# Kernel tuning notes

Hardware: AMD Instinct MI355X
Metric: run time of the kernel (lower is better)

The kernel has to match this reference:

```python
import jax, jax.numpy as jnp
import numpy as np

# Dimensions
B, D1, D2 = 256, 68, 3          # inputs: [B, 68 landmarks, 3 coords]
OUT = D1 * D2                   # output_size = 204
H = 1024                        # hidden_size
NUM_CLASSES = 12
LENGTH = 128                    # decoded sequence length
NUM_LAYERS = 3
IN0 = OUT + NUM_CLASSES         # LSTM layer-0 input size = 216


def setup_inputs() -> dict:
    key = jax.random.key(0)
    ks = jax.random.split(key, 32)
    s = 0.02

    def rn(k, shape):
        return (jax.random.normal(k, shape, jnp.float32) * s)

    inp = {
        "inputs": jax.random.normal(ks[0], (B, D1, D2), jnp.float32),
        # LSTM layer 0 (input size IN0), layers 1,2 (input size H). Gate order: i,f,g,o.
        "W_ih0": rn(ks[1], (IN0, 4 * H)), "W_hh0": rn(ks[2], (H, 4 * H)),
        "b_ih0": rn(ks[3], (4 * H,)),     "b_hh0": rn(ks[4], (4 * H,)),
        "W_ih1": rn(ks[5], (H, 4 * H)),   "W_hh1": rn(ks[6], (H, 4 * H)),
        "b_ih1": rn(ks[7], (4 * H,)),     "b_hh1": rn(ks[8], (4 * H,)),
        "W_ih2": rn(ks[9], (H, 4 * H)),   "W_hh2": rn(ks[10], (H, 4 * H)),
        "b_ih2": rn(ks[11], (4 * H,)),    "b_hh2": rn(ks[12], (4 * H,)),
        # fc head: hidden -> output_size
        "fc_W": rn(ks[13], (H, OUT)), "fc_b": rn(ks[14], (OUT,)),
        # state initializers: output_size -> 3*hidden
        "inh_W": rn(ks[15], (OUT, 3 * H)), "inh_b": rn(ks[16], (3 * H,)),
        "inc_W": rn(ks[17], (OUT, 3 * H)), "inc_b": rn(ks[18], (3 * H,)),
        "labels": 5,  # scalar class id
    }
    return inp


def _lstm_cell(x, h, c, W_ih, W_hh, b_ih, b_hh):
    gates = x @ W_ih + h @ W_hh + (b_ih + b_hh)        # [B, 4H]
    i, f, g, o = jnp.split(gates, 4, axis=-1)
    i = jax.nn.sigmoid(i)
    f = jax.nn.sigmoid(f)
    g = jnp.tanh(g)
    o = jax.nn.sigmoid(o)
    c2 = f * c + i * g
    h2 = o * jnp.tanh(c2)
    return h2, c2


def reference(inputs, W_ih0, W_hh0, b_ih0, b_hh0,
              W_ih1, W_hh1, b_ih1, b_hh1,
              W_ih2, W_hh2, b_ih2, b_hh2,
              fc_W, fc_b, inh_W, inh_b, inc_W, inc_b, labels):
    b, d1, d2 = inputs.shape
    frame = inputs.reshape(b, d1 * d2)                              # [B, OUT]
    # init states, reshaped (B, 3, H) -> (layers, B, H)
    h0 = (frame @ inh_W + inh_b).reshape(b, NUM_LAYERS, H).transpose(1, 0, 2)
    c0 = (frame @ inc_W + inc_b).reshape(b, NUM_LAYERS, H).transpose(1, 0, 2)
    enc = jax.nn.one_hot(jnp.asarray(labels), NUM_CLASSES, dtype=frame.dtype)
    x_in = jnp.concatenate([frame, jnp.broadcast_to(enc, (b, NUM_CLASSES))], axis=-1)  # [B, IN0]

    layers = ((W_ih0, W_hh0, b_ih0, b_hh0),
              (W_ih1, W_hh1, b_ih1, b_hh1),
              (W_ih2, W_hh2, b_ih2, b_hh2))

    def step(carry, _):
        h, c = carry                                                # each [3, B, H]
        x = x_in
        hs, cs = [], []
        for l in range(NUM_LAYERS):
            hn, cn = _lstm_cell(x, h[l], c[l], *layers[l])
            hs.append(hn)
            cs.append(cn)
            x = hn
        out = x @ fc_W + fc_b                                       # [B, OUT]
        return (jnp.stack(hs), jnp.stack(cs)), out

    (_, _), outs = jax.lax.scan(step, (h0, c0), None, length=LENGTH)  # [L, B, OUT]
    return outs.transpose(1, 0, 2).reshape(b, LENGTH, d1, d2)
```

## Files before the change

kernel.cpp:

```cpp
#include <hip/hip_runtime.h>


#define DEVINL static __device__ __forceinline__

typedef __bf16 bf16x8 __attribute__((ext_vector_type(8)));
typedef float f32x4 __attribute__((ext_vector_type(4)));
typedef unsigned short u16;
typedef unsigned int u32;

DEVINL u16 f2bf(float f) {
  u32 u = __builtin_bit_cast(u32, f);
  u += 0x7fffu + ((u >> 16) & 1u);
  return (u16)(u >> 16);
}
DEVINL float bf2f(u16 h) {
  u32 u = (u32)h << 16;
  return __builtin_bit_cast(float, u);
}
DEVINL float sigm(float x) { return 1.0f / (1.0f + __expf(-x)); }
DEVINL float tanhfast(float x) { return 1.0f - 2.0f / (1.0f + __expf(2.0f * x)); }

DEVINL void glds_coh(const u16* g, u16* l) {
  __builtin_amdgcn_global_load_lds(
      (const __attribute__((address_space(1))) u32*)g,
      (__attribute__((address_space(3))) u32*)l, 16, 0, 17);
}
DEVINL void glds(const u16* g, u16* l) {
  __builtin_amdgcn_global_load_lds(
      (const __attribute__((address_space(1))) u32*)g,
      (__attribute__((address_space(3))) u32*)l, 16, 0, 0);
}

DEVINL int permcol(int P) {
  int grp = P >> 6, g = (P >> 4) & 3, jj = P & 15;
  return g * 1024 + grp * 16 + jj;
}

struct Params {
  const float* fc_b;
  const float* inh_b;
  const float* inc_b;
  const u16 *WT0, *WT1, *WT2, *WT00, *FCW, *WIH, *WIC, *FRB;
  u16* HB;
  u16* G0P;
  float *G0B, *B1P, *B2P, *CC;
  float* out;
};

#define MODE_L0 0
#define MODE_L 1
#define MODE_FC 2
#define MODE_G0 3
#define MODE_H 4
#define MODE_C 5

DEVINL void issue_tile(int kt, const u16* A0, const u16* A1, int kSplit, int sA,
                       int K, const u16* Wt, int m0, int wrow,
                       const int (&rq)[4], const int (&kqs)[4],
                       const int (&lo)[4], u16* Abuf, u16* Bbuf) {
  const u16* Ab = (kt < kSplit) ? (A0 + kt) : (A1 + (kt - kSplit));
#pragma unroll
  for (int q = 0; q < 4; ++q)
    glds_coh(Ab + (size_t)(m0 + rq[q]) * sA + kqs[q] * 8, Abuf + lo[q]);
  const u16* Bb = Wt + kt;
#pragma unroll
  for (int q = 0; q < 2; ++q)
    glds(Bb + (size_t)(wrow + rq[q]) * K + kqs[q] * 8, Bbuf + lo[q]);
}

DEVINL void mfma_tile(const u16* Al, const u16* Bl, f32x4 (&acc)[2][4], int rl0,
                      int hh, int e7, int jj) {
#pragma unroll
  for (int kk = 0; kk < 2; ++kk) {
    int sl = (((kk << 2) | hh) ^ e7) * 8;
    bf16x8 a0 = *(const bf16x8*)(Al + rl0 * 64 + sl);
    bf16x8 a1 = *(const bf16x8*)(Al + (rl0 + 16) * 64 + sl);
    bf16x8 b0 = *(const bf16x8*)(Bl + (jj)*64 + sl);
    bf16x8 b1 = *(const bf16x8*)(Bl + (16 + jj) * 64 + sl);
    bf16x8 b2 = *(const bf16x8*)(Bl + (32 + jj) * 64 + sl);
    bf16x8 b3 = *(const bf16x8*)(Bl + (48 + jj) * 64 + sl);
    acc[0][0] = __builtin_amdgcn_mfma_f32_16x16x32_bf16(a0, b0, acc[0][0], 0, 0, 0);
    acc[0][1] = __builtin_amdgcn_mfma_f32_16x16x32_bf16(a0, b1, acc[0][1], 0, 0, 0);
    acc[0][2] = __builtin_amdgcn_mfma_f32_16x16x32_bf16(a0, b2, acc[0][2], 0, 0, 0);
    acc[0][3] = __builtin_amdgcn_mfma_f32_16x16x32_bf16(a0, b3, acc[0][3], 0, 0, 0);
    acc[1][0] = __builtin_amdgcn_mfma_f32_16x16x32_bf16(a1, b0, acc[1][0], 0, 0, 0);
    acc[1][1] = __builtin_amdgcn_mfma_f32_16x16x32_bf16(a1, b1, acc[1][1], 0, 0, 0);
    acc[1][2] = __builtin_amdgcn_mfma_f32_16x16x32_bf16(a1, b2, acc[1][2], 0, 0, 0);
    acc[1][3] = __builtin_amdgcn_mfma_f32_16x16x32_bf16(a1, b3, acc[1][3], 0, 0, 0);
  }
}

template <int MODE>
DEVINL void mm_body(u16* Al, u16* Bl, const u16* A0, const u16* A1, int sA,
                    int kSplit, int K, const u16* Wt, int m0, int bn, int t,
                    const u16* Gfull, const float* biasP, float* Cst, u16* Hout,
                    float* outp) {
  const int tid = threadIdx.x;
  const int l = tid & 63;
  const int w = tid >> 6;
  const int hh = (l >> 4) & 3;
  const int jj = l & 15;
  const int rl0 = w * 32 + jj;
  const int e7 = l & 7;

  int rq[4], kqs[4], lo[4];
#pragma unroll
  for (int q = 0; q < 4; ++q) {
    int L = tid + q * 256;
    rq[q] = L >> 3;
    kqs[q] = (L & 7) ^ (rq[q] & 7);
    lo[q] = ((tid & ~63) + q * 256) * 8;
  }

  f32x4 acc[2][4];
#pragma unroll
  for (int m = 0; m < 2; ++m)
#pragma unroll
    for (int g = 0; g < 4; ++g) acc[m][g] = (f32x4){0.f, 0.f, 0.f, 0.f};

  const int wrow = bn * 64;
  const int n = K >> 6;

  issue_tile(0, A0, A1, kSplit, sA, K, Wt, m0, wrow, rq, kqs, lo, Al, Bl);
  issue_tile(64, A0, A1, kSplit, sA, K, Wt, m0, wrow, rq, kqs, lo, Al + 8192,
             Bl + 4096);

  for (int j = 0; j < n; ++j) {
    u16* Ac = Al + (j & 1) * 8192;
    u16* Bc = Bl + (j & 1) * 4096;
    if (j < n - 1)
      asm volatile("s_waitcnt vmcnt(6)" ::: "memory");
    else
      asm volatile("s_waitcnt vmcnt(0)" ::: "memory");
    __builtin_amdgcn_s_barrier();
    __builtin_amdgcn_sched_barrier(0);
    mfma_tile(Ac, Bc, acc, rl0, hh, e7, jj);
    __builtin_amdgcn_sched_barrier(0);
    __builtin_amdgcn_s_barrier();
    if (j + 2 < n)
      issue_tile((j + 2) * 64, A0, A1, kSplit, sA, K, Wt, m0, wrow, rq, kqs, lo,
                 Ac, Bc);
  }

  const int rb = m0 + w * 32 + (hh << 2);
  if (MODE <= MODE_L) {
    float add0 = 0.f, add1 = 0.f, add2 = 0.f, add3 = 0.f;
    if (MODE == MODE_L) {
      add0 = biasP[bn * 64 + jj];
      add1 = biasP[bn * 64 + 16 + jj];
      add2 = biasP[bn * 64 + 32 + jj];
      add3 = biasP[bn * 64 + 48 + jj];
    }
    const int j = bn * 16 + jj;
#pragma unroll
    for (int m = 0; m < 2; ++m) {
#pragma unroll
      for (int r = 0; r < 4; ++r) {
        int b = rb + m * 16 + r;
        float g0v, g1v, g2v, g3v;
        if (MODE == MODE_L0) {
          const u16* G = Gfull + (size_t)b * 4096 + bn * 64 + jj;
          g0v = acc[m][0][r] + bf2f(G[0]);
          g1v = acc[m][1][r] + bf2f(G[16]);
          g2v = acc[m][2][r] + bf2f(G[32]);
          g3v = acc[m][3][r] + bf2f(G[48]);
        } else {
          g0v = acc[m][0][r] + add0;
          g1v = acc[m][1][r] + add1;
          g2v = acc[m][2][r] + add2;
          g3v = acc[m][3][r] + add3;
        }
        float iv = sigm(g0v), fv = sigm(g1v), gv = tanhfast(g2v), ov = sigm(g3v);
        size_t ci = (size_t)b * 1024 + j;
        float cn = fv * Cst[ci] + iv * gv;
        Cst[ci] = cn;
        Hout[ci] = f2bf(ov * tanhfast(cn));
      }
    }
  } else if (MODE == MODE_FC) {
#pragma unroll
    for (int g = 0; g < 4; ++g) {
      int nn = bn * 64 + g * 16 + jj;
      if (nn < 204) {
        float bv2 = biasP[nn];
#pragma unroll
        for (int m = 0; m < 2; ++m)
#pragma unroll
          for (int r = 0; r < 4; ++r) {
            int b = rb + m * 16 + r;
            outp[((size_t)b * 128 + t) * 204 + nn] = acc[m][g][r] + bv2;
          }
      }
    }
  } else if (MODE == MODE_G0) {
#pragma unroll
    for (int g = 0; g < 4; ++g) {
      int P = bn * 64 + g * 16 + jj;
      float bv2 = biasP[P];
#pragma unroll
      for (int m = 0; m < 2; ++m)
#pragma unroll
        for (int r = 0; r < 4; ++r) {
          int b = rb + m * 16 + r;
          Hout[(size_t)b * 4096 + P] = f2bf(acc[m][g][r] + bv2);
        }
    }
  } else {
#pragma unroll
    for (int g = 0; g < 4; ++g) {
      int nn = bn * 64 + g * 16 + jj;
      int lay = nn >> 10, j2 = nn & 1023;
      float bv2 = biasP[nn];
#pragma unroll
      for (int m = 0; m < 2; ++m)
#pragma unroll
        for (int r = 0; r < 4; ++r) {
          int b = rb + m * 16 + r;
          float v = acc[m][g][r] + bv2;
          if (MODE == MODE_H)
            Hout[(size_t)((lay * 2 + 1) * 256 + b) * 1024 + j2] = f2bf(v);
          else
            outp[(size_t)(lay * 256 + b) * 1024 + j2] = v;
        }
    }
  }
}

DEVINL void grid_barrier(u32* bar, int bid, int ep) {
  __syncthreads();
  if (threadIdx.x == 0) {
    __builtin_amdgcn_fence(__ATOMIC_RELEASE, "agent");
    __hip_atomic_fetch_add(bar + (bid & 7) * 64, 1u, __ATOMIC_RELAXED,
                           __HIP_MEMORY_SCOPE_AGENT);
    if (bid == 0) {
#pragma unroll 1
      for (int g = 0; g < 8; ++g)
        while (__hip_atomic_load(bar + g * 64, __ATOMIC_RELAXED,
                                 __HIP_MEMORY_SCOPE_AGENT) < (u32)ep * 49u)
          __builtin_amdgcn_s_sleep(8);
      __hip_atomic_store(bar + 512, (u32)ep, __ATOMIC_RELAXED,
                         __HIP_MEMORY_SCOPE_AGENT);
    } else {
#pragma unroll 1
      while (__hip_atomic_load(bar + 512, __ATOMIC_RELAXED,
                               __HIP_MEMORY_SCOPE_AGENT) < (u32)ep)
        __builtin_amdgcn_s_sleep(8);
    }
  }
  __syncthreads();
}

__global__ __launch_bounds__(256, 2) void persist_kernel(Params p, u32* bar) {
  __shared__ u16 Al[2 * 128 * 64];
  __shared__ u16 Bl[2 * 64 * 64];
  const int bid = blockIdx.x;
  int job, mb, bn;
  if (bid < 384) {
    job = bid >> 7;
    int r = bid & 127;
    bn = (r & 7) * 8 + (r >> 4);
    mb = (r >> 3) & 1;
  } else {
    job = 3;
    int r = bid - 384;
    mb = r >> 2;
    bn = r & 3;
  }
  u16* HB = p.HB;
#define HBP(lay, pp) (HB + (size_t)(((lay)*2 + (pp)) * 256) * 1024)
  for (int i = 0; i <= 130; ++i) {
    int t = i - job;
    if ((unsigned)t < 128u) {
      int par = t & 1, pv = par ^ 1;
      if (job == 0) {
        mm_body<MODE_L0>(Al, Bl, HBP(0, pv), nullptr, 1024, 1 << 30, 1024,
                         p.WT0, mb * 128, bn, t, p.G0P, nullptr, p.CC,
                         HBP(0, par), nullptr);
      } else if (job == 1) {
        mm_body<MODE_L>(Al, Bl, HBP(0, par), HBP(1, pv), 1024, 1024, 2048,
                        p.WT1, mb * 128, bn, t, nullptr, p.B1P,
                        p.CC + (size_t)256 * 1024, HBP(1, par), nullptr);
      } else if (job == 2) {
        mm_body<MODE_L>(Al, Bl, HBP(1, par), HBP(2, pv), 1024, 1024, 2048,
                        p.WT2, mb * 128, bn, t, nullptr, p.B2P,
                        p.CC + (size_t)512 * 1024, HBP(2, par), nullptr);
      } else {
        mm_body<MODE_FC>(Al, Bl, HBP(2, par), nullptr, 1024, 1 << 30, 1024,
                         p.FCW, mb * 128, bn, t, nullptr, p.fc_b, nullptr,
                         nullptr, p.out);
      }
    }
    if (i < 130) grid_barrier(bar, bid, i + 1);
  }
#undef HBP
}

__global__ __launch_bounds__(256, 2) void setup_mm(Params p) {
  __shared__ u16 Al[2 * 128 * 64];
  __shared__ u16 Bl[2 * 64 * 64];
  int bid = blockIdx.x;
  if (bid < 128) {
    mm_body<MODE_G0>(Al, Bl, p.FRB, nullptr, 256, 1 << 30, 256, p.WT00,
                     (bid >> 6) * 128, bid & 63, 0, nullptr, p.G0B, nullptr,
                     p.G0P, nullptr);
  } else if (bid < 224) {
    int b2 = bid - 128;
    mm_body<MODE_H>(Al, Bl, p.FRB, nullptr, 256, 1 << 30, 256, p.WIH,
                    (b2 / 48) * 128, b2 % 48, 0, nullptr, p.inh_b, nullptr,
                    p.HB, nullptr);
  } else {
    int b2 = bid - 224;
    mm_body<MODE_C>(Al, Bl, p.FRB, nullptr, 256, 1 << 30, 256, p.WIC,
                    (b2 / 48) * 128, b2 % 48, 0, nullptr, p.inc_b, nullptr,
                    nullptr, p.CC);
  }
}

__global__ __launch_bounds__(256) void transpose_bf16(
    const float* __restrict__ srcA, const float* __restrict__ srcB,
    int srcStride, int kSplit, int Kvalid, int Nvalid, int perm,
    u16* __restrict__ dst, int Ktot) {
  __shared__ float tile[64][17];
  int P0 = blockIdx.x * 16;
  int k0 = blockIdx.y * 64;
  int t = threadIdx.x;
  int nl = t & 15;
  int kh = t >> 4;
  int P = P0 + nl;
  int n = perm ? permcol(P) : P;
  bool nok = (n < Nvalid);
#pragma unroll
  for (int q = 0; q < 4; ++q) {
    int kl = q * 16 + kh;
    int k = k0 + kl;
    float v = 0.f;
    if (nok && k < Kvalid) {
      const float* s = (k < kSplit) ? (srcA + (size_t)k * srcStride)
                                    : (srcB + (size_t)(k - kSplit) * srcStride);
      v = s[n];
    }
    tile[kl][nl] = v;
  }
  __syncthreads();
  int jo = t >> 4;
  int kb = (t & 15) << 2;
  unsigned long long pk =
      (unsigned long long)f2bf(tile[kb + 0][jo]) |
      ((unsigned long long)f2bf(tile[kb + 1][jo]) << 16) |
      ((unsigned long long)f2bf(tile[kb + 2][jo]) << 32) |
      ((unsigned long long)f2bf(tile[kb + 3][jo]) << 48);
  *(unsigned long long*)(dst + (size_t)(P0 + jo) * Ktot + k0 + kb) = pk;
}

__global__ __launch_bounds__(256) void build_frame(const float* __restrict__ inputs,
                                                   u16* __restrict__ FRB) {
  int id = blockIdx.x * 256 + threadIdx.x;
  int b = id >> 8, k = id & 255;
  FRB[id] = (k < 204) ? f2bf(inputs[b * 204 + k]) : (u16)0;
}

__global__ __launch_bounds__(256) void build_bias(
    const float* __restrict__ W_ih0, const float* __restrict__ b_ih0,
    const float* __restrict__ b_hh0, const float* __restrict__ b_ih1,
    const float* __restrict__ b_hh1, const float* __restrict__ b_ih2,
    const float* __restrict__ b_hh2, const int* __restrict__ labels,
    float* __restrict__ G0B, float* __restrict__ B1P, float* __restrict__ B2P) {
  int P = blockIdx.x * 256 + threadIdx.x;
  int n = permcol(P);
  int lab = labels[0];
  G0B[P] = W_ih0[(size_t)(204 + lab) * 4096 + n] + b_ih0[n] + b_hh0[n];
  B1P[P] = b_ih1[n] + b_hh1[n];
  B2P[P] = b_ih2[n] + b_hh2[n];
}

extern "C" void kernel_launch(void* const* d_in, const int* in_sizes, int n_in,
                              void* d_out, int out_size, void* d_ws,
                              size_t ws_size, hipStream_t stream) {
  const float* inputs = (const float*)d_in[0];
  const float* W_ih0 = (const float*)d_in[1];
  const float* W_hh0 = (const float*)d_in[2];
  const float* b_ih0 = (const float*)d_in[3];
  const float* b_hh0 = (const float*)d_in[4];
  const float* W_ih1 = (const float*)d_in[5];
  const float* W_hh1 = (const float*)d_in[6];
  const float* b_ih1 = (const float*)d_in[7];
  const float* b_hh1 = (const float*)d_in[8];
  const float* W_ih2 = (const float*)d_in[9];
  const float* W_hh2 = (const float*)d_in[10];
  const float* b_ih2 = (const float*)d_in[11];
  const float* b_hh2 = (const float*)d_in[12];
  const float* fc_W = (const float*)d_in[13];
  const float* fc_b = (const float*)d_in[14];
  const float* inh_W = (const float*)d_in[15];
  const float* inh_b = (const float*)d_in[16];
  const float* inc_W = (const float*)d_in[17];
  const float* inc_b = (const float*)d_in[18];
  const int* labels = (const int*)d_in[19];

  char* ws = (char*)d_ws;
  size_t off = 0;
  auto alloc = [&](size_t bytes) {
    void* r = ws + off;
    off = (off + bytes + 255) & ~(size_t)255;
    return r;
  };
  u16* WT0 = (u16*)alloc(4096ull * 1024 * 2);
  u16* WT1 = (u16*)alloc(4096ull * 2048 * 2);
  u16* WT2 = (u16*)alloc(4096ull * 2048 * 2);
  u16* WT00 = (u16*)alloc(4096ull * 256 * 2);
  u16* FCW = (u16*)alloc(256ull * 1024 * 2);
  u16* WIH = (u16*)alloc(3072ull * 256 * 2);
  u16* WIC = (u16*)alloc(3072ull * 256 * 2);
  u16* FRB = (u16*)alloc(256ull * 256 * 2);
  u16* HB = (u16*)alloc(3ull * 2 * 256 * 1024 * 2);
  u16* G0P = (u16*)alloc(256ull * 4096 * 2);
  float* G0B = (float*)alloc(4096ull * 4);
  float* B1P = (float*)alloc(4096ull * 4);
  float* B2P = (float*)alloc(4096ull * 4);
  float* CC = (float*)alloc(3ull * 256 * 1024 * 4);
  u32* BAR = (u32*)alloc(4096);
  if (off > ws_size) return;

  const int BIG = 1 << 30;
  transpose_bf16<<<dim3(256, 16), 256, 0, stream>>>(W_hh0, nullptr, 4096, BIG, 1024, 4096, 1, WT0, 1024);
  transpose_bf16<<<dim3(256, 32), 256, 0, stream>>>(W_ih1, W_hh1, 4096, 1024, 2048, 4096, 1, WT1, 2048);
  transpose_bf16<<<dim3(256, 32), 256, 0, stream>>>(W_ih2, W_hh2, 4096, 1024, 2048, 4096, 1, WT2, 2048);
  transpose_bf16<<<dim3(256, 4), 256, 0, stream>>>(W_ih0, nullptr, 4096, BIG, 204, 4096, 1, WT00, 256);
  transpose_bf16<<<dim3(16, 16), 256, 0, stream>>>(fc_W, nullptr, 204, BIG, 1024, 204, 0, FCW, 1024);
  transpose_bf16<<<dim3(192, 4), 256, 0, stream>>>(inh_W, nullptr, 3072, BIG, 204, 3072, 0, WIH, 256);
  transpose_bf16<<<dim3(192, 4), 256, 0, stream>>>(inc_W, nullptr, 3072, BIG, 204, 3072, 0, WIC, 256);
  build_frame<<<256, 256, 0, stream>>>(inputs, FRB);
  build_bias<<<16, 256, 0, stream>>>(W_ih0, b_ih0, b_hh0, b_ih1, b_hh1, b_ih2,
                                     b_hh2, labels, G0B, B1P, B2P);
  hipMemsetAsync(BAR, 0, 4096, stream);

  Params p;
  p.fc_b = fc_b; p.inh_b = inh_b; p.inc_b = inc_b;
  p.WT0 = WT0; p.WT1 = WT1; p.WT2 = WT2; p.WT00 = WT00; p.FCW = FCW;
  p.WIH = WIH; p.WIC = WIC; p.FRB = FRB; p.HB = HB;
  p.G0P = G0P; p.G0B = G0B; p.B1P = B1P; p.B2P = B2P; p.CC = CC;
  p.out = (float*)d_out;

  setup_mm<<<320, 256, 0, stream>>>(p);

  persist_kernel<<<392, 256, 0, stream>>>(p, BAR);
}
```

Before: 5.285 ms.

## Mirror hidden states per XCD so GEMM A-loads hit local L2

Each XCD's blocks first copy the full previous-step hidden-state buffers (all three layers) into a private per-XCD mirror, using coherent atomic loads, and then sync with a new XCD-local barrier. The GEMM A-operand loads then read from the mirror through cacheable loads instead of the system-coherent loads used before. The aim is to avoid slow cross-XCD coherent traffic on the repeated A-tile reads. The cost is an extra copy of about 1.5MB per XCD every step, an extra barrier per step, and dependence on the hardware XCC id register for grouping blocks.

```diff
diff --git a/kernel.cpp b/kernel.cpp
--- a/kernel.cpp
+++ b/kernel.cpp
@@ -7,6 +7,7 @@
 typedef float f32x4 __attribute__((ext_vector_type(4)));
 typedef unsigned short u16;
 typedef unsigned int u32;
+typedef unsigned long long u64;
 
 DEVINL u16 f2bf(float f) {
   u32 u = __builtin_bit_cast(u32, f);
@@ -20,12 +21,12 @@
 DEVINL float sigm(float x) { return 1.0f / (1.0f + __expf(-x)); }
 DEVINL float tanhfast(float x) { return 1.0f - 2.0f / (1.0f + __expf(2.0f * x)); }
 
-DEVINL void glds_coh(const u16* g, u16* l) {
+DEVINL void glds_a(const u16* g, u16* l) {
   __builtin_amdgcn_global_load_lds(
       (const __attribute__((address_space(1))) u32*)g,
-      (__attribute__((address_space(3))) u32*)l, 16, 0, 17);
-}
-DEVINL void glds(const u16* g, u16* l) {
+      (__attribute__((address_space(3))) u32*)l, 16, 0, 1);
+}
+DEVINL void glds_w(const u16* g, u16* l) {
   __builtin_amdgcn_global_load_lds(
       (const __attribute__((address_space(1))) u32*)g,
       (__attribute__((address_space(3))) u32*)l, 16, 0, 0);
@@ -42,6 +43,7 @@
   const float* inc_b;
   const u16 *WT0, *WT1, *WT2, *WT00, *FCW, *WIH, *WIC, *FRB;
   u16* HB;
+  u16* HM;
   u16* G0P;
   float *G0B, *B1P, *B2P, *CC;
   float* out;
@@ -61,11 +63,11 @@
   const u16* Ab = (kt < kSplit) ? (A0 + kt) : (A1 + (kt - kSplit));
 #pragma unroll
   for (int q = 0; q < 4; ++q)
-    glds_coh(Ab + (size_t)(m0 + rq[q]) * sA + kqs[q] * 8, Abuf + lo[q]);
+    glds_a(Ab + (size_t)(m0 + rq[q]) * sA + kqs[q] * 8, Abuf + lo[q]);
   const u16* Bb = Wt + kt;
 #pragma unroll
   for (int q = 0; q < 2; ++q)
-    glds(Bb + (size_t)(wrow + rq[q]) * K + kqs[q] * 8, Bbuf + lo[q]);
+    glds_w(Bb + (size_t)(wrow + rq[q]) * K + kqs[q] * 8, Bbuf + lo[q]);
 }
 
 DEVINL void mfma_tile(const u16* Al, const u16* Bl, f32x4 (&acc)[2][4], int rl0,
@@ -250,9 +252,37 @@
   __syncthreads();
 }
 
+DEVINL void xcd_barrier(u32* ctr, int nb, int ep) {
+  __syncthreads();
+  if (threadIdx.x == 0) {
+    __hip_atomic_fetch_add(ctr, 1u, __ATOMIC_RELAXED, __HIP_MEMORY_SCOPE_AGENT);
+#pragma unroll 1
+    while (__hip_atomic_load(ctr, __ATOMIC_RELAXED, __HIP_MEMORY_SCOPE_AGENT) <
+           (u32)ep * (u32)nb)
+      __builtin_amdgcn_s_sleep(4);
+  }
+  __syncthreads();
+}
+
+DEVINL void pull_mirror(const u16* HB, u16* HMx, int i, int rank, int nb) {
+  const int total = 3 * 65536;
+  const int stride = nb * 256;
+  u64* dst = (u64*)HMx;
+#pragma unroll 4
+  for (int c = rank * 256 + threadIdx.x; c < total; c += stride) {
+    int lyr = c >> 16, off = c & 65535;
+    int pl = (i - 1 - lyr) & 1;
+    const u64* s = (const u64*)(HB + ((size_t)(lyr * 2 + pl) << 18));
+    u64 v = __hip_atomic_load(s + off, __ATOMIC_RELAXED,
+                              __HIP_MEMORY_SCOPE_AGENT);
+    dst[c] = v;
+  }
+}
+
 __global__ __launch_bounds__(256, 2) void persist_kernel(Params p, u32* bar) {
   __shared__ u16 Al[2 * 128 * 64];
   __shared__ u16 Bl[2 * 64 * 64];
+  __shared__ int sh_x, sh_rank, sh_nb;
   const int bid = blockIdx.x;
   int job, mb, bn;
   if (bid < 384) {
@@ -266,31 +296,57 @@
     mb = r >> 2;
     bn = r & 3;
   }
+
+  if (threadIdx.x == 0) {
+    int x = __builtin_amdgcn_s_getreg((31 << 11) | 20) & 7;
+    sh_x = x;
+    sh_rank = (int)__hip_atomic_fetch_add(bar + 1024 + x * 64, 1u,
+                                          __ATOMIC_RELAXED,
+                                          __HIP_MEMORY_SCOPE_AGENT);
+  }
+  __syncthreads();
+  const int x = sh_x, rank = sh_rank;
+  grid_barrier(bar, bid, 1);
+  if (threadIdx.x == 0)
+    sh_nb = (int)__hip_atomic_load(bar + 1024 + x * 64, __ATOMIC_RELAXED,
+                                   __HIP_MEMORY_SCOPE_AGENT);
+  __syncthreads();
+  const int nb = sh_nb;
+  u16* HMx = p.HM + ((size_t)(x * 3) << 18);
+  u32* xctr = bar + 2048 + x * 64;
+
+  pull_mirror(p.HB, HMx, 0, rank, nb);
+  xcd_barrier(xctr, nb, 1);
+
   u16* HB = p.HB;
-#define HBP(lay, pp) (HB + (size_t)(((lay)*2 + (pp)) * 256) * 1024)
+#define HBP(lay, pp) (HB + (size_t)(((lay)*2 + (pp)) << 18))
   for (int i = 0; i <= 130; ++i) {
     int t = i - job;
     if ((unsigned)t < 128u) {
-      int par = t & 1, pv = par ^ 1;
+      int par = t & 1;
       if (job == 0) {
-        mm_body<MODE_L0>(Al, Bl, HBP(0, pv), nullptr, 1024, 1 << 30, 1024,
-                         p.WT0, mb * 128, bn, t, p.G0P, nullptr, p.CC,
-                         HBP(0, par), nullptr);
+        mm_body<MODE_L0>(Al, Bl, HMx, nullptr, 1024, 1 << 30, 1024, p.WT0,
+                         mb * 128, bn, t, p.G0P, nullptr, p.CC, HBP(0, par),
+                         nullptr);
       } else if (job == 1) {
-        mm_body<MODE_L>(Al, Bl, HBP(0, par), HBP(1, pv), 1024, 1024, 2048,
-                        p.WT1, mb * 128, bn, t, nullptr, p.B1P,
+        mm_body<MODE_L>(Al, Bl, HMx, HMx + (1 << 18), 1024, 1024, 2048, p.WT1,
+                        mb * 128, bn, t, nullptr, p.B1P,
                         p.CC + (size_t)256 * 1024, HBP(1, par), nullptr);
       } else if (job == 2) {
-        mm_body<MODE_L>(Al, Bl, HBP(1, par), HBP(2, pv), 1024, 1024, 2048,
-                        p.WT2, mb * 128, bn, t, nullptr, p.B2P,
+        mm_body<MODE_L>(Al, Bl, HMx + (1 << 18), HMx + (2 << 18), 1024, 1024,
+                        2048, p.WT2, mb * 128, bn, t, nullptr, p.B2P,
                         p.CC + (size_t)512 * 1024, HBP(2, par), nullptr);
       } else {
-        mm_body<MODE_FC>(Al, Bl, HBP(2, par), nullptr, 1024, 1 << 30, 1024,
+        mm_body<MODE_FC>(Al, Bl, HMx + (2 << 18), nullptr, 1024, 1 << 30, 1024,
                          p.FCW, mb * 128, bn, t, nullptr, p.fc_b, nullptr,
                          nullptr, p.out);
       }
     }
-    if (i < 130) grid_barrier(bar, bid, i + 1);
+    if (i < 130) {
+      grid_barrier(bar, bid, i + 2);
+      pull_mirror(p.HB, HMx, i + 1, rank, nb);
+      xcd_barrier(xctr, nb, i + 2);
+    }
   }
 #undef HBP
 }
@@ -344,12 +400,10 @@
   __syncthreads();
   int jo = t >> 4;
   int kb = (t & 15) << 2;
-  unsigned long long pk =
-      (unsigned long long)f2bf(tile[kb + 0][jo]) |
-      ((unsigned long long)f2bf(tile[kb + 1][jo]) << 16) |
-      ((unsigned long long)f2bf(tile[kb + 2][jo]) << 32) |
-      ((unsigned long long)f2bf(tile[kb + 3][jo]) << 48);
-  *(unsigned long long*)(dst + (size_t)(P0 + jo) * Ktot + k0 + kb) = pk;
+  u64 pk = (u64)f2bf(tile[kb + 0][jo]) | ((u64)f2bf(tile[kb + 1][jo]) << 16) |
+           ((u64)f2bf(tile[kb + 2][jo]) << 32) |
+           ((u64)f2bf(tile[kb + 3][jo]) << 48);
+  *(u64*)(dst + (size_t)(P0 + jo) * Ktot + k0 + kb) = pk;
 }
 
 __global__ __launch_bounds__(256) void build_frame(const float* __restrict__ inputs,
@@ -413,12 +467,13 @@
   u16* WIC = (u16*)alloc(3072ull * 256 * 2);
   u16* FRB = (u16*)alloc(256ull * 256 * 2);
   u16* HB = (u16*)alloc(3ull * 2 * 256 * 1024 * 2);
+  u16* HM = (u16*)alloc(8ull * 3 * 256 * 1024 * 2);
   u16* G0P = (u16*)alloc(256ull * 4096 * 2);
   float* G0B = (float*)alloc(4096ull * 4);
   float* B1P = (float*)alloc(4096ull * 4);
   float* B2P = (float*)alloc(4096ull * 4);
   float* CC = (float*)alloc(3ull * 256 * 1024 * 4);
-  u32* BAR = (u32*)alloc(4096);
+  u32* BAR = (u32*)alloc(16384);
   if (off > ws_size) return;
 
   const int BIG = 1 << 30;
@@ -432,12 +487,12 @@
   build_frame<<<256, 256, 0, stream>>>(inputs, FRB);
   build_bias<<<16, 256, 0, stream>>>(W_ih0, b_ih0, b_hh0, b_ih1, b_hh1, b_ih2,
                                      b_hh2, labels, G0B, B1P, B2P);
-  hipMemsetAsync(BAR, 0, 4096, stream);
+  hipMemsetAsync(BAR, 0, 16384, stream);
 
   Params p;
   p.fc_b = fc_b; p.inh_b = inh_b; p.inc_b = inc_b;
   p.WT0 = WT0; p.WT1 = WT1; p.WT2 = WT2; p.WT00 = WT00; p.FCW = FCW;
-  p.WIH = WIH; p.WIC = WIC; p.FRB = FRB; p.HB = HB;
+  p.WIH = WIH; p.WIC = WIC; p.FRB = FRB; p.HB = HB; p.HM = HM;
   p.G0P = G0P; p.G0B = G0B; p.B1P = B1P; p.B2P = B2P; p.CC = CC;
   p.out = (float*)d_out;
 
```

Result: slower. 7.067 ms (+33.7%).

## Use 512-thread blocks with 16-row waves and triple-buffered LDS pipeline

Applied to the files above, without the earlier changes.

Doubles threads per block so each wave computes a 16-row slice instead of 32, and moves the global-to-LDS pipeline from double to triple buffering with adjusted vmcnt waits. The aim is more latency hiding and deeper prefetch in the latency-bound persistent recurrent kernel. In exchange it raises LDS use per block and reduces per-wave MFMA reuse of B fragments, which may limit occupancy.

```diff
diff --git a/kernel.cpp b/kernel.cpp
--- a/kernel.cpp
+++ b/kernel.cpp
@@ -7,6 +7,7 @@
 typedef float f32x4 __attribute__((ext_vector_type(4)));
 typedef unsigned short u16;
 typedef unsigned int u32;
+typedef unsigned long long u64;
 
 DEVINL u16 f2bf(float f) {
   u32 u = __builtin_bit_cast(u32, f);
@@ -25,7 +26,7 @@
       (const __attribute__((address_space(1))) u32*)g,
       (__attribute__((address_space(3))) u32*)l, 16, 0, 17);
 }
-DEVINL void glds(const u16* g, u16* l) {
+DEVINL void glds_w(const u16* g, u16* l) {
   __builtin_amdgcn_global_load_lds(
       (const __attribute__((address_space(1))) u32*)g,
       (__attribute__((address_space(3))) u32*)l, 16, 0, 0);
@@ -54,39 +55,35 @@
 #define MODE_H 4
 #define MODE_C 5
 
+#define ABUF 8192
+#define BBUF 4096
+
 DEVINL void issue_tile(int kt, const u16* A0, const u16* A1, int kSplit, int sA,
                        int K, const u16* Wt, int m0, int wrow,
-                       const int (&rq)[4], const int (&kqs)[4],
-                       const int (&lo)[4], u16* Abuf, u16* Bbuf) {
+                       const int (&rqA)[2], const int (&kqA)[2],
+                       const int (&loA)[2], int rqB, int kqB, int loB,
+                       u16* Abuf, u16* Bbuf) {
   const u16* Ab = (kt < kSplit) ? (A0 + kt) : (A1 + (kt - kSplit));
 #pragma unroll
-  for (int q = 0; q < 4; ++q)
-    glds_coh(Ab + (size_t)(m0 + rq[q]) * sA + kqs[q] * 8, Abuf + lo[q]);
-  const u16* Bb = Wt + kt;
-#pragma unroll
   for (int q = 0; q < 2; ++q)
-    glds(Bb + (size_t)(wrow + rq[q]) * K + kqs[q] * 8, Bbuf + lo[q]);
-}
-
-DEVINL void mfma_tile(const u16* Al, const u16* Bl, f32x4 (&acc)[2][4], int rl0,
+    glds_coh(Ab + (size_t)(m0 + rqA[q]) * sA + kqA[q] * 8, Abuf + loA[q]);
+  glds_w(Wt + kt + (size_t)(wrow + rqB) * K + kqB * 8, Bbuf + loB);
+}
+
+DEVINL void mfma_tile(const u16* Al, const u16* Bl, f32x4 (&acc)[4], int rl0,
                       int hh, int e7, int jj) {
 #pragma unroll
   for (int kk = 0; kk < 2; ++kk) {
     int sl = (((kk << 2) | hh) ^ e7) * 8;
     bf16x8 a0 = *(const bf16x8*)(Al + rl0 * 64 + sl);
-    bf16x8 a1 = *(const bf16x8*)(Al + (rl0 + 16) * 64 + sl);
     bf16x8 b0 = *(const bf16x8*)(Bl + (jj)*64 + sl);
     bf16x8 b1 = *(const bf16x8*)(Bl + (16 + jj) * 64 + sl);
     bf16x8 b2 = *(const bf16x8*)(Bl + (32 + jj) * 64 + sl);
     bf16x8 b3 = *(const bf16x8*)(Bl + (48 + jj) * 64 + sl);
-    acc[0][0] = __builtin_amdgcn_mfma_f32_16x16x32_bf16(a0, b0, acc[0][0], 0, 0, 0);
-    acc[0][1] = __builtin_amdgcn_mfma_f32_16x16x32_bf16(a0, b1, acc[0][1], 0, 0, 0);
-    acc[0][2] = __builtin_amdgcn_mfma_f32_16x16x32_bf16(a0, b2, acc[0][2], 0, 0, 0);
-    acc[0][3] = __builtin_amdgcn_mfma_f32_16x16x32_bf16(a0, b3, acc[0][3], 0, 0, 0);
-    acc[1][0] = __builtin_amdgcn_mfma_f32_16x16x32_bf16(a1, b0, acc[1][0], 0, 0, 0);
-    acc[1][1] = __builtin_amdgcn_mfma_f32_16x16x32_bf16(a1, b1, acc[1][1], 0, 0, 0);
-    acc[1][2] = __builtin_amdgcn_mfma_f32_16x16x32_bf16(a1, b2, acc[1][2], 0, 0, 0);
-    acc[1][3] = __builtin_amdgcn_mfma_f32_16x16x32_bf16(a1, b3, acc[1][3], 0, 0, 0);
+    acc[0] = __builtin_amdgcn_mfma_f32_16x16x32_bf16(a0, b0, acc[0], 0, 0, 0);
+    acc[1] = __builtin_amdgcn_mfma_f32_16x16x32_bf16(a0, b1, acc[1], 0, 0, 0);
+    acc[2] = __builtin_amdgcn_mfma_f32_16x16x32_bf16(a0, b2, acc[2], 0, 0, 0);
+    acc[3] = __builtin_amdgcn_mfma_f32_16x16x32_bf16(a0, b3, acc[3], 0, 0, 0);
   }
 }
 
@@ -100,36 +97,43 @@
   const int w = tid >> 6;
   const int hh = (l >> 4) & 3;
   const int jj = l & 15;
-  const int rl0 = w * 32 + jj;
+  const int rl0 = w * 16 + jj;
   const int e7 = l & 7;
 
-  int rq[4], kqs[4], lo[4];
-#pragma unroll
-  for (int q = 0; q < 4; ++q) {
-    int L = tid + q * 256;
-    rq[q] = L >> 3;
-    kqs[q] = (L & 7) ^ (rq[q] & 7);
-    lo[q] = ((tid & ~63) + q * 256) * 8;
-  }
-
-  f32x4 acc[2][4];
-#pragma unroll
-  for (int m = 0; m < 2; ++m)
-#pragma unroll
-    for (int g = 0; g < 4; ++g) acc[m][g] = (f32x4){0.f, 0.f, 0.f, 0.f};
+  int rqA[2], kqA[2], loA[2];
+#pragma unroll
+  for (int q = 0; q < 2; ++q) {
+    int L = tid + q * 512;
+    rqA[q] = L >> 3;
+    kqA[q] = (L & 7) ^ (rqA[q] & 7);
+    loA[q] = ((tid & ~63) + q * 512) * 8;
+  }
+  const int rqB = tid >> 3;
+  const int kqB = (tid & 7) ^ (rqB & 7);
+  const int loB = (tid & ~63) * 8;
+
+  f32x4 acc[4];
+#pragma unroll
+  for (int g = 0; g < 4; ++g) acc[g] = (f32x4){0.f, 0.f, 0.f, 0.f};
 
   const int wrow = bn * 64;
   const int n = K >> 6;
 
-  issue_tile(0, A0, A1, kSplit, sA, K, Wt, m0, wrow, rq, kqs, lo, Al, Bl);
-  issue_tile(64, A0, A1, kSplit, sA, K, Wt, m0, wrow, rq, kqs, lo, Al + 8192,
-             Bl + 4096);
+  issue_tile(0, A0, A1, kSplit, sA, K, Wt, m0, wrow, rqA, kqA, loA, rqB, kqB,
+             loB, Al, Bl);
+  issue_tile(64, A0, A1, kSplit, sA, K, Wt, m0, wrow, rqA, kqA, loA, rqB, kqB,
+             loB, Al + ABUF, Bl + BBUF);
+  issue_tile(128, A0, A1, kSplit, sA, K, Wt, m0, wrow, rqA, kqA, loA, rqB, kqB,
+             loB, Al + 2 * ABUF, Bl + 2 * BBUF);
 
   for (int j = 0; j < n; ++j) {
-    u16* Ac = Al + (j & 1) * 8192;
-    u16* Bc = Bl + (j & 1) * 4096;
-    if (j < n - 1)
+    int s = j % 3;
+    u16* Ac = Al + s * ABUF;
+    u16* Bc = Bl + s * BBUF;
+    if (j <= n - 3)
       asm volatile("s_waitcnt vmcnt(6)" ::: "memory");
+    else if (j == n - 2)
+      asm volatile("s_waitcnt vmcnt(3)" ::: "memory");
     else
       asm volatile("s_waitcnt vmcnt(0)" ::: "memory");
     __builtin_amdgcn_s_barrier();
@@ -137,12 +141,12 @@
     mfma_tile(Ac, Bc, acc, rl0, hh, e7, jj);
     __builtin_amdgcn_sched_barrier(0);
     __builtin_amdgcn_s_barrier();
-    if (j + 2 < n)
-      issue_tile((j + 2) * 64, A0, A1, kSplit, sA, K, Wt, m0, wrow, rq, kqs, lo,
-                 Ac, Bc);
-  }
-
-  const int rb = m0 + w * 32 + (hh << 2);
+    if (j + 3 < n)
+      issue_tile((j + 3) * 64, A0, A1, kSplit, sA, K, Wt, m0, wrow, rqA, kqA,
+                 loA, rqB, kqB, loB, Ac, Bc);
+  }
+
+  const int rb = m0 + w * 16 + (hh << 2);
   if (MODE <= MODE_L) {
     float add0 = 0.f, add1 = 0.f, add2 = 0.f, add3 = 0.f;
     if (MODE == MODE_L) {
@@ -153,29 +157,26 @@
     }
     const int j = bn * 16 + jj;
 #pragma unroll
-    for (int m = 0; m < 2; ++m) {
-#pragma unroll
-      for (int r = 0; r < 4; ++r) {
-        int b = rb + m * 16 + r;
-        float g0v, g1v, g2v, g3v;
-        if (MODE == MODE_L0) {
-          const u16* G = Gfull + (size_t)b * 4096 + bn * 64 + jj;
-          g0v = acc[m][0][r] + bf2f(G[0]);
-          g1v = acc[m][1][r] + bf2f(G[16]);
-          g2v = acc[m][2][r] + bf2f(G[32]);
-          g3v = acc[m][3][r] + bf2f(G[48]);
-        } else {
-          g0v = acc[m][0][r] + add0;
-          g1v = acc[m][1][r] + add1;
-          g2v = acc[m][2][r] + add2;
-          g3v = acc[m][3][r] + add3;
-        }
-        float iv = sigm(g0v), fv = sigm(g1v), gv = tanhfast(g2v), ov = sigm(g3v);
-        size_t ci = (size_t)b * 1024 + j;
-        float cn = fv * Cst[ci] + iv * gv;
-        Cst[ci] = cn;
-        Hout[ci] = f2bf(ov * tanhfast(cn));
+    for (int r = 0; r < 4; ++r) {
+      int b = rb + r;
+      float g0v, g1v, g2v, g3v;
+      if (MODE == MODE_L0) {
+        const u16* G = Gfull + (size_t)b * 4096 + bn * 64 + jj;
+        g0v = acc[0][r] + bf2f(G[0]);
+        g1v = acc[1][r] + bf2f(G[16]);
+        g2v = acc[2][r] + bf2f(G[32]);
+        g3v = acc[3][r] + bf2f(G[48]);
+      } else {
+        g0v = acc[0][r] + add0;
+        g1v = acc[1][r] + add1;
+        g2v = acc[2][r] + add2;
+        g3v = acc[3][r] + add3;
       }
+      float iv = sigm(g0v), fv = sigm(g1v), gv = tanhfast(g2v), ov = sigm(g3v);
+      size_t ci = (size_t)b * 1024 + j;
+      float cn = fv * Cst[ci] + iv * gv;
+      Cst[ci] = cn;
+      Hout[ci] = f2bf(ov * tanhfast(cn));
     }
   } else if (MODE == MODE_FC) {
 #pragma unroll
@@ -184,12 +185,10 @@
       if (nn < 204) {
         float bv2 = biasP[nn];
 #pragma unroll
-        for (int m = 0; m < 2; ++m)
-#pragma unroll
-          for (int r = 0; r < 4; ++r) {
-            int b = rb + m * 16 + r;
-            outp[((size_t)b * 128 + t) * 204 + nn] = acc[m][g][r] + bv2;
-          }
+        for (int r = 0; r < 4; ++r) {
+          int b = rb + r;
+          outp[((size_t)b * 128 + t) * 204 + nn] = acc[g][r] + bv2;
+        }
       }
     }
   } else if (MODE == MODE_G0) {
@@ -198,12 +197,10 @@
       int P = bn * 64 + g * 16 + jj;
       float bv2 = biasP[P];
 #pragma unroll
-      for (int m = 0; m < 2; ++m)
-#pragma unroll
-        for (int r = 0; r < 4; ++r) {
-          int b = rb + m * 16 + r;
-          Hout[(size_t)b * 4096 + P] = f2bf(acc[m][g][r] + bv2);
-        }
+      for (int r = 0; r < 4; ++r) {
+        int b = rb + r;
+        Hout[(size_t)b * 4096 + P] = f2bf(acc[g][r] + bv2);
+      }
     }
   } else {
 #pragma unroll
@@ -212,16 +209,14 @@
       int lay = nn >> 10, j2 = nn & 1023;
       float bv2 = biasP[nn];
 #pragma unroll
-      for (int m = 0; m < 2; ++m)
-#pragma unroll
-        for (int r = 0; r < 4; ++r) {
-          int b = rb + m * 16 + r;
-          float v = acc[m][g][r] + bv2;
-          if (MODE == MODE_H)
-            Hout[(size_t)((lay * 2 + 1) * 256 + b) * 1024 + j2] = f2bf(v);
-          else
-            outp[(size_t)(lay * 256 + b) * 1024 + j2] = v;
-        }
+      for (int r = 0; r < 4; ++r) {
+        int b = rb + r;
+        float v = acc[g][r] + bv2;
+        if (MODE == MODE_H)
+          Hout[(size_t)((lay * 2 + 1) * 256 + b) * 1024 + j2] = f2bf(v);
+        else
+          outp[(size_t)(lay * 256 + b) * 1024 + j2] = v;
+      }
     }
   }
 }
@@ -250,9 +245,9 @@
   __syncthreads();
 }
 
-__global__ __launch_bounds__(256, 2) void persist_kernel(Params p, u32* bar) {
-  __shared__ u16 Al[2 * 128 * 64];
-  __shared__ u16 Bl[2 * 64 * 64];
+__global__ __launch_bounds__(512, 4) void persist_kernel(Params p, u32* bar) {
+  __shared__ u16 Al[3 * ABUF];
+  __shared__ u16 Bl[3 * BBUF];
   const int bid = blockIdx.x;
   int job, mb, bn;
   if (bid < 384) {
@@ -267,7 +262,7 @@
     bn = r & 3;
   }
   u16* HB = p.HB;
-#define HBP(lay, pp) (HB + (size_t)(((lay)*2 + (pp)) * 256) * 1024)
+#define HBP(lay, pp) (HB + (size_t)(((lay)*2 + (pp)) << 18))
   for (int i = 0; i <= 130; ++i) {
     int t = i - job;
     if ((unsigned)t < 128u) {
@@ -295,9 +290,9 @@
 #undef HBP
 }
 
-__global__ __launch_bounds__(256, 2) void setup_mm(Params p) {
-  __shared__ u16 Al[2 * 128 * 64];
-  __shared__ u16 Bl[2 * 64 * 64];
+__global__ __launch_bounds__(512, 4) void setup_mm(Params p) {
+  __shared__ u16 Al[3 * ABUF];
+  __shared__ u16 Bl[3 * BBUF];
   int bid = blockIdx.x;
   if (bid < 128) {
     mm_body<MODE_G0>(Al, Bl, p.FRB, nullptr, 256, 1 << 30, 256, p.WT00,
@@ -344,12 +339,10 @@
   __syncthreads();
   int jo = t >> 4;
   int kb = (t & 15) << 2;
-  unsigned long long pk =
-      (unsigned long long)f2bf(tile[kb + 0][jo]) |
-      ((unsigned long long)f2bf(tile[kb + 1][jo]) << 16) |
-      ((unsigned long long)f2bf(tile[kb + 2][jo]) << 32) |
-      ((unsigned long long)f2bf(tile[kb + 3][jo]) << 48);
-  *(unsigned long long*)(dst + (size_t)(P0 + jo) * Ktot + k0 + kb) = pk;
+  u64 pk = (u64)f2bf(tile[kb + 0][jo]) | ((u64)f2bf(tile[kb + 1][jo]) << 16) |
+           ((u64)f2bf(tile[kb + 2][jo]) << 32) |
+           ((u64)f2bf(tile[kb + 3][jo]) << 48);
+  *(u64*)(dst + (size_t)(P0 + jo) * Ktot + k0 + kb) = pk;
 }
 
 __global__ __launch_bounds__(256) void build_frame(const float* __restrict__ inputs,
@@ -441,7 +434,7 @@
   p.G0P = G0P; p.G0B = G0B; p.B1P = B1P; p.B2P = B2P; p.CC = CC;
   p.out = (float*)d_out;
 
-  setup_mm<<<320, 256, 0, stream>>>(p);
-
-  persist_kernel<<<392, 256, 0, stream>>>(p, BAR);
-}
+  setup_mm<<<320, 512, 0, stream>>>(p);
+
+  persist_kernel<<<392, 512, 0, stream>>>(p, BAR);
+}
```

After: 5.470 ms. +3.5%, slower.

## Stream part of LSTM weight tiles with nontemporal loads; parallelize barrier polling

Applied to the files above, without the earlier changes.

Blocks whose bn&7 is at least 5 now load their weight tiles with a nontemporal cache policy (aux=2). The likely aim is to keep the rest of the weight working set resident in the shared cache across the 128 recurrent steps instead of having it thrashed. The grid barrier's master block now polls the eight counter groups with eight threads in parallel and a shorter sleep, instead of one thread checking them in sequence. Both changes touch cache behaviour and barrier latency, and the partial-NT split is a heuristic that could shift misses onto other blocks.

```diff
diff --git a/kernel.cpp b/kernel.cpp
--- a/kernel.cpp
+++ b/kernel.cpp
@@ -7,6 +7,7 @@
 typedef float f32x4 __attribute__((ext_vector_type(4)));
 typedef unsigned short u16;
 typedef unsigned int u32;
+typedef unsigned long long u64;
 
 DEVINL u16 f2bf(float f) {
   u32 u = __builtin_bit_cast(u32, f);
@@ -25,10 +26,15 @@
       (const __attribute__((address_space(1))) u32*)g,
       (__attribute__((address_space(3))) u32*)l, 16, 0, 17);
 }
-DEVINL void glds(const u16* g, u16* l) {
+DEVINL void glds_w(const u16* g, u16* l) {
   __builtin_amdgcn_global_load_lds(
       (const __attribute__((address_space(1))) u32*)g,
       (__attribute__((address_space(3))) u32*)l, 16, 0, 0);
+}
+DEVINL void glds_wnt(const u16* g, u16* l) {
+  __builtin_amdgcn_global_load_lds(
+      (const __attribute__((address_space(1))) u32*)g,
+      (__attribute__((address_space(3))) u32*)l, 16, 0, 2);
 }
 
 DEVINL int permcol(int P) {
@@ -57,15 +63,21 @@
 DEVINL void issue_tile(int kt, const u16* A0, const u16* A1, int kSplit, int sA,
                        int K, const u16* Wt, int m0, int wrow,
                        const int (&rq)[4], const int (&kqs)[4],
-                       const int (&lo)[4], u16* Abuf, u16* Bbuf) {
+                       const int (&lo)[4], u16* Abuf, u16* Bbuf, int nt) {
   const u16* Ab = (kt < kSplit) ? (A0 + kt) : (A1 + (kt - kSplit));
 #pragma unroll
   for (int q = 0; q < 4; ++q)
     glds_coh(Ab + (size_t)(m0 + rq[q]) * sA + kqs[q] * 8, Abuf + lo[q]);
   const u16* Bb = Wt + kt;
-#pragma unroll
-  for (int q = 0; q < 2; ++q)
-    glds(Bb + (size_t)(wrow + rq[q]) * K + kqs[q] * 8, Bbuf + lo[q]);
+  if (nt) {
+#pragma unroll
+    for (int q = 0; q < 2; ++q)
+      glds_wnt(Bb + (size_t)(wrow + rq[q]) * K + kqs[q] * 8, Bbuf + lo[q]);
+  } else {
+#pragma unroll
+    for (int q = 0; q < 2; ++q)
+      glds_w(Bb + (size_t)(wrow + rq[q]) * K + kqs[q] * 8, Bbuf + lo[q]);
+  }
 }
 
 DEVINL void mfma_tile(const u16* Al, const u16* Bl, f32x4 (&acc)[2][4], int rl0,
@@ -94,7 +106,7 @@
 DEVINL void mm_body(u16* Al, u16* Bl, const u16* A0, const u16* A1, int sA,
                     int kSplit, int K, const u16* Wt, int m0, int bn, int t,
                     const u16* Gfull, const float* biasP, float* Cst, u16* Hout,
-                    float* outp) {
+                    float* outp, int nt) {
   const int tid = threadIdx.x;
   const int l = tid & 63;
   const int w = tid >> 6;
@@ -121,9 +133,9 @@
   const int wrow = bn * 64;
   const int n = K >> 6;
 
-  issue_tile(0, A0, A1, kSplit, sA, K, Wt, m0, wrow, rq, kqs, lo, Al, Bl);
+  issue_tile(0, A0, A1, kSplit, sA, K, Wt, m0, wrow, rq, kqs, lo, Al, Bl, nt);
   issue_tile(64, A0, A1, kSplit, sA, K, Wt, m0, wrow, rq, kqs, lo, Al + 8192,
-             Bl + 4096);
+             Bl + 4096, nt);
 
   for (int j = 0; j < n; ++j) {
     u16* Ac = Al + (j & 1) * 8192;
@@ -139,7 +151,7 @@
     __builtin_amdgcn_s_barrier();
     if (j + 2 < n)
       issue_tile((j + 2) * 64, A0, A1, kSplit, sA, K, Wt, m0, wrow, rq, kqs, lo,
-                 Ac, Bc);
+                 Ac, Bc, nt);
   }
 
   const int rb = m0 + w * 32 + (hh << 2);
@@ -228,24 +240,31 @@
 
 DEVINL void grid_barrier(u32* bar, int bid, int ep) {
   __syncthreads();
-  if (threadIdx.x == 0) {
+  const int tid = threadIdx.x;
+  if (bid == 0) {
+    if (tid == 0) {
+      __builtin_amdgcn_fence(__ATOMIC_RELEASE, "agent");
+      __hip_atomic_fetch_add(bar, 1u, __ATOMIC_RELAXED,
+                             __HIP_MEMORY_SCOPE_AGENT);
+    }
+    if (tid < 8) {
+#pragma unroll 1
+      while (__hip_atomic_load(bar + tid * 64, __ATOMIC_RELAXED,
+                               __HIP_MEMORY_SCOPE_AGENT) < (u32)ep * 49u)
+        __builtin_amdgcn_s_sleep(4);
+    }
+    __syncthreads();
+    if (tid == 0)
+      __hip_atomic_store(bar + 512, (u32)ep, __ATOMIC_RELAXED,
+                         __HIP_MEMORY_SCOPE_AGENT);
+  } else if (tid == 0) {
     __builtin_amdgcn_fence(__ATOMIC_RELEASE, "agent");
     __hip_atomic_fetch_add(bar + (bid & 7) * 64, 1u, __ATOMIC_RELAXED,
                            __HIP_MEMORY_SCOPE_AGENT);
-    if (bid == 0) {
 #pragma unroll 1
-      for (int g = 0; g < 8; ++g)
-        while (__hip_atomic_load(bar + g * 64, __ATOMIC_RELAXED,
-                                 __HIP_MEMORY_SCOPE_AGENT) < (u32)ep * 49u)
-          __builtin_amdgcn_s_sleep(8);
-      __hip_atomic_store(bar + 512, (u32)ep, __ATOMIC_RELAXED,
-                         __HIP_MEMORY_SCOPE_AGENT);
-    } else {
-#pragma unroll 1
-      while (__hip_atomic_load(bar + 512, __ATOMIC_RELAXED,
-                               __HIP_MEMORY_SCOPE_AGENT) < (u32)ep)
-        __builtin_amdgcn_s_sleep(8);
-    }
+    while (__hip_atomic_load(bar + 512, __ATOMIC_RELAXED,
+                             __HIP_MEMORY_SCOPE_AGENT) < (u32)ep)
+      __builtin_amdgcn_s_sleep(8);
   }
   __syncthreads();
 }
@@ -266,8 +285,9 @@
     mb = r >> 2;
     bn = r & 3;
   }
+  const int nt = (bid < 384) && ((bn & 7) >= 5);
   u16* HB = p.HB;
-#define HBP(lay, pp) (HB + (size_t)(((lay)*2 + (pp)) * 256) * 1024)
+#define HBP(lay, pp) (HB + (size_t)(((lay)*2 + (pp)) << 18))
   for (int i = 0; i <= 130; ++i) {
     int t = i - job;
     if ((unsigned)t < 128u) {
@@ -275,19 +295,19 @@
       if (job == 0) {
         mm_body<MODE_L0>(Al, Bl, HBP(0, pv), nullptr, 1024, 1 << 30, 1024,
                          p.WT0, mb * 128, bn, t, p.G0P, nullptr, p.CC,
-                         HBP(0, par), nullptr);
+                         HBP(0, par), nullptr, nt);
       } else if (job == 1) {
         mm_body<MODE_L>(Al, Bl, HBP(0, par), HBP(1, pv), 1024, 1024, 2048,
                         p.WT1, mb * 128, bn, t, nullptr, p.B1P,
-                        p.CC + (size_t)256 * 1024, HBP(1, par), nullptr);
+                        p.CC + (size_t)256 * 1024, HBP(1, par), nullptr, nt);
       } else if (job == 2) {
         mm_body<MODE_L>(Al, Bl, HBP(1, par), HBP(2, pv), 1024, 1024, 2048,
                         p.WT2, mb * 128, bn, t, nullptr, p.B2P,
-                        p.CC + (size_t)512 * 1024, HBP(2, par), nullptr);
+                        p.CC + (size_t)512 * 1024, HBP(2, par), nullptr, nt);
       } else {
         mm_body<MODE_FC>(Al, Bl, HBP(2, par), nullptr, 1024, 1 << 30, 1024,
                          p.FCW, mb * 128, bn, t, nullptr, p.fc_b, nullptr,
-                         nullptr, p.out);
+                         nullptr, p.out, nt);
       }
     }
     if (i < 130) grid_barrier(bar, bid, i + 1);
@@ -302,17 +322,17 @@
   if (bid < 128) {
     mm_body<MODE_G0>(Al, Bl, p.FRB, nullptr, 256, 1 << 30, 256, p.WT00,
                      (bid >> 6) * 128, bid & 63, 0, nullptr, p.G0B, nullptr,
-                     p.G0P, nullptr);
+                     p.G0P, nullptr, 0);
   } else if (bid < 224) {
     int b2 = bid - 128;
     mm_body<MODE_H>(Al, Bl, p.FRB, nullptr, 256, 1 << 30, 256, p.WIH,
                     (b2 / 48) * 128, b2 % 48, 0, nullptr, p.inh_b, nullptr,
-                    p.HB, nullptr);
+                    p.HB, nullptr, 0);
   } else {
     int b2 = bid - 224;
     mm_body<MODE_C>(Al, Bl, p.FRB, nullptr, 256, 1 << 30, 256, p.WIC,
                     (b2 / 48) * 128, b2 % 48, 0, nullptr, p.inc_b, nullptr,
-                    nullptr, p.CC);
+                    nullptr, p.CC, 0);
   }
 }
 
@@ -344,12 +364,10 @@
   __syncthreads();
   int jo = t >> 4;
   int kb = (t & 15) << 2;
-  unsigned long long pk =
-      (unsigned long long)f2bf(tile[kb + 0][jo]) |
-      ((unsigned long long)f2bf(tile[kb + 1][jo]) << 16) |
-      ((unsigned long long)f2bf(tile[kb + 2][jo]) << 32) |
-      ((unsigned long long)f2bf(tile[kb + 3][jo]) << 48);
-  *(unsigned long long*)(dst + (size_t)(P0 + jo) * Ktot + k0 + kb) = pk;
+  u64 pk = (u64)f2bf(tile[kb + 0][jo]) | ((u64)f2bf(tile[kb + 1][jo]) << 16) |
+           ((u64)f2bf(tile[kb + 2][jo]) << 32) |
+           ((u64)f2bf(tile[kb + 3][jo]) << 48);
+  *(u64*)(dst + (size_t)(P0 + jo) * Ktot + k0 + kb) = pk;
 }
 
 __global__ __launch_bounds__(256) void build_frame(const float* __restrict__ inputs,
```

Result: slower. 6.116 ms (+15.7%).
